# Kernel optimization log

Hardware: AMD Instinct MI355X
Metric: run time of the kernel (lower is better)

Reference implementation:

```python
import jax, jax.numpy as jnp
import numpy as np

# ---- static config (matches module defaults / init_kwargs) ----
SX = 256; SY = 256; C = 3; NK = 12; B = 4
R = 10; DT = 0.2; DD = 5; SIGMA = 0.65; THETA_A = 1.0; N_EXP = 2


def _build_kernels():
    """Replicates compute_kernel(): multi-ring Lenia kernels, normalized in real space."""
    rng = np.random.default_rng(42)
    mid = SX // 2
    g = np.mgrid[-mid:mid, -mid:mid]
    dist = np.linalg.norm(g, axis=0)  # [SX, SY]
    Ks = []
    for _ in range(NK):
        r = rng.uniform(0.3, 1.0)
        a = rng.uniform(0.0, 1.0, 3)
        w = rng.uniform(0.05, 0.2, 3)
        b = rng.uniform(0.0, 1.0, 3)
        D = dist / ((R + 15) * r)
        sig = 1.0 / (1.0 + np.exp((D - 1.0) * 10.0))  # sigmoid(-(D-1)*10)
        kerf = (b[None, None, :] * np.exp(-(((D[..., None] - a[None, None, :]) / w[None, None, :]) ** 2) / 2.0)).sum(-1)
        Ks.append(sig * kerf)
    K = np.stack(Ks, axis=-1)  # [SX, SY, NK]
    Kn = K / K.sum(axis=(0, 1), keepdims=True)
    m = rng.uniform(0.05, 0.5, NK)
    s = rng.uniform(0.01, 0.18, NK)
    h = rng.uniform(0.2, 1.0, NK)
    return (Kn.astype(np.float32), m.astype(np.float32), s.astype(np.float32), h.astype(np.float32))


def setup_inputs() -> dict:
    key = jax.random.key(0)
    Kn, m, s, h = _build_kernels()
    A = jax.random.uniform(key, (B, 1, SX, SY, C), dtype=jnp.float32)
    c0 = jnp.asarray(np.arange(NK) % C, dtype=jnp.int32)      # source channel of each kernel
    c1_map = jnp.asarray(np.arange(NK) % C, dtype=jnp.int32)  # target channel of each kernel
    return {"A": A, "Kn": jnp.asarray(Kn), "m": jnp.asarray(m), "s": jnp.asarray(s),
            "h": jnp.asarray(h), "c0": c0, "c1_map": c1_map}


def _sobel(A):
    """Circular (torus) Sobel, separable [1,2,1]x[-1,0,1]/8, on spatial axes (2,3).
    A: [B,1,SX,SY,C] -> [B,1,SX,SY,2,C] (d/dx, d/dy)."""
    sy = jnp.roll(A, -1, 3) + 2.0 * A + jnp.roll(A, 1, 3)
    gx = (jnp.roll(sy, -1, 2) - jnp.roll(sy, 1, 2)) / 8.0
    sx = jnp.roll(A, -1, 2) + 2.0 * A + jnp.roll(A, 1, 2)
    gy = (jnp.roll(sx, -1, 3) - jnp.roll(sx, 1, 3)) / 8.0
    return jnp.stack([gx, gy], axis=4)


def _forward(A, Kn, m, s, h, c0, c1_map):
    # FFT-domain convolution per kernel
    fK = jnp.fft.fft2(jnp.fft.fftshift(Kn, axes=(0, 1)), axes=(0, 1))  # [SX,SY,NK] complex
    fA = jnp.fft.fft2(A, axes=(2, 3))                                   # [B,1,SX,SY,C]
    fAk = fA[..., c0]                                                    # [B,1,SX,SY,NK]
    U = jnp.fft.ifft2(fK[None, None] * fAk, axes=(2, 3)).real           # [B,1,SX,SY,NK]
    # growth(U,m,s) = 2*bell(U,m,s)-1, scaled by h
    G = (2.0 * jnp.exp(-((U - m) ** 2) / (2.0 * s ** 2)) - 1.0) * h
    # sum kernel contributions into their target channel (c1)
    M = jax.nn.one_hot(c1_map, C, dtype=G.dtype)                         # [NK,C]
    Uc = jnp.einsum('bzxyk,kc->bzxyc', G, M)                             # [B,1,SX,SY,C]
    nabla_U = _sobel(Uc)                                                 # [B,1,SX,SY,2,C]
    nabla_A = _sobel(A.sum(-1, keepdims=True))                           # [B,1,SX,SY,2,1]
    alpha = jnp.clip((A[:, :, :, :, None, :] / THETA_A) ** N_EXP, 0.0, 1.0)
    F = nabla_U * (1.0 - alpha) - nabla_A * alpha                        # flow field
    # ---- reintegration tracking (RT) over a (2*DD+1)^2 neighborhood ----
    x = jnp.arange(SX, dtype=F.dtype); y = jnp.arange(SY, dtype=F.dtype)
    pos = jnp.stack(jnp.meshgrid(x, y, indexing='ij'), axis=-1) + 0.5    # [SX,SY,2]
    ma = DD - SIGMA
    mus = pos[None, None, :, :, :, None] + jnp.clip(DT * F, -ma, ma)     # target centers [B,1,SX,SY,2,C]
    offsets = jnp.asarray([(dx, dy) for dx in range(-DD, DD + 1) for dy in range(-DD, DD + 1)], dtype=jnp.int32)
    amax = min(1.0, 2.0 * SIGMA)

    def body(acc, off):
        dx, dy = off[0], off[1]
        rollA = jnp.roll(A, (dx, dy), axis=(2, 3))
        rollmu = jnp.roll(mus, (dx, dy), axis=(2, 3))
        dpmu = jnp.abs(pos[None, None, :, :, :, None] - rollmu)
        sz = 0.5 - dpmu + SIGMA
        area = jnp.prod(jnp.clip(sz, 0.0, amax), axis=4) / (4.0 * SIGMA ** 2)  # [B,1,SX,SY,C]
        return acc + rollA * area, None

    nA, _ = jax.lax.scan(jax.checkpoint(body), jnp.zeros_like(A), offsets)
    return nA


def reference(A, Kn, m, s, h, c0, c1_map):
    return _forward(A, Kn, m, s, h, c0, c1_map)
```

## Files before the change

### kernel.cpp

```cpp
#include <hip/hip_runtime.h>


typedef _Float16 f16;
typedef __attribute__((ext_vector_type(8))) _Float16 half8;
typedef __attribute__((ext_vector_type(16))) float f32x16;

#define RMAX 44
#define NROWS 89
#define NDMAX 8
#define NFRAG (3*NROWS*NDMAX)
#define NBPK ((NFRAG + 4) / 4)
#define ST 168
#define TROWS 120
#define SCHED_STRIDE 1024
#define KTHR 1e-7f

__global__ __launch_bounds__(128) void lenia_meta(const float* __restrict__ Kn,
                                                  int2* __restrict__ meta,
                                                  int* __restrict__ rowr) {
    int blk = blockIdx.x;
    int c = blk / NROWS, ri = blk - c * NROWS;
    int di = ri - RMAX;
    int t = threadIdx.x;
    int dj = t - RMAX;
    int act = 0;
    if (t < NROWS) {
        size_t base = (size_t)(((di + 128) << 8) | (dj + 128)) * 12 + c;
        float k0 = Kn[base], k1 = Kn[base + 3], k2 = Kn[base + 6], k3 = Kn[base + 9];
        act = (fmaxf(fmaxf(k0, k1), fmaxf(k2, k3)) > KTHR) ? 1 : 0;
    }
    __shared__ int smn[128], smx[128];
    smn[t] = act ? dj : 1000;
    smx[t] = act ? dj : -1000;
    __syncthreads();
    for (int s = 64; s > 0; s >>= 1) {
        if (t < s) { smn[t] = min(smn[t], smn[t + s]); smx[t] = max(smx[t], smx[t + s]); }
        __syncthreads();
    }
    if (t == 0) {
        int jmn = smn[0], jmx = smx[0];
        if (jmx < jmn) { meta[blk] = make_int2(1, 0); rowr[blk] = 0; }
        else {
            meta[blk] = make_int2(jmn, jmx);
            rowr[blk] = max(abs(di), max(abs(jmn), abs(jmx)));
        }
    }
}

__global__ __launch_bounds__(128) void lenia_sched(const int2* __restrict__ meta,
                                                   const int* __restrict__ rowr,
                                                   int2* __restrict__ meta2,
                                                   unsigned int* __restrict__ sched,
                                                   int* __restrict__ nsched,
                                                   int* __restrict__ radii) {
    int c = blockIdx.x;
    int t = threadIdx.x;
    __shared__ int pre[NROWS], nds[NROWS], rmx[128];
    int nd = 0, d0 = 0;
    if (t < NROWS) {
        int2 bm = meta[c * NROWS + t];
        if (bm.y >= bm.x) {
            d0 = ((bm.x - 7) >> 3) << 3;
            nd = ((bm.y + 7 - d0) >> 4) + 1;
        }
        meta2[c * NROWS + t] = make_int2(d0, nd);
        nds[t] = nd;
    }
    rmx[t] = (t < NROWS) ? rowr[c * NROWS + t] : 0;
    __syncthreads();
    for (int s = 64; s > 0; s >>= 1) {
        if (t < s) rmx[t] = max(rmx[t], rmx[t + s]);
        __syncthreads();
    }
    __shared__ int tot;
    if (t == 0) {
        radii[c] = rmx[0];
        int acc = 0;
        for (int i = 0; i < NROWS; ++i) { pre[i] = acc; acc += nds[i]; }
        tot = acc;
    }
    __syncthreads();
    if (t < NROWS && nd > 0) {
        int base = pre[t];
        for (int i = 0; i < nd; ++i) {
            int delta = d0 + 16 * i;
            unsigned int off = (unsigned int)(t * ST + delta + 128);
            sched[c * SCHED_STRIDE + base + i] =
                (unsigned int)((c * NROWS + t) * NDMAX + i) | (off << 12);
        }
    }
    if (t == 0) {
        int ns = (tot + 31) & ~31;
        unsigned int padoff = (unsigned int)(RMAX * ST + 128);
        for (int i = tot; i < ns + 48; ++i)
            sched[c * SCHED_STRIDE + i] = (unsigned int)NFRAG | (padoff << 12);
        nsched[c] = ns;
    }
}

__global__ __launch_bounds__(256) void lenia_prep2(const float* __restrict__ Kn,
                                                   const float* __restrict__ A,
                                                   const int2* __restrict__ meta2,
                                                   uint4* __restrict__ bpack,
                                                   f16* __restrict__ Atr) {
    int blk = blockIdx.x;
    if (blk < NBPK) {
        int fi = blk * 4 + (threadIdx.x >> 6);
        int l = threadIdx.x & 63;
        if (fi > NFRAG) return;
        union { f16 h[8]; uint4 u; } pk;
        if (fi == NFRAG) {
            pk.u = make_uint4(0, 0, 0, 0);
            bpack[(size_t)fi * 64 + l] = pk.u;
            return;
        }
        int c = fi / (NROWS * NDMAX);
        int rem = fi - c * (NROWS * NDMAX);
        int ri = rem >> 3, didx = rem & 7;
        int di = ri - RMAX;
        int delta = meta2[c * NROWS + ri].x + 16 * didx;
        int q = (l & 31) >> 3, sy = l & 7, g = l >> 5;
        int dj0 = delta + 8 * g - sy;
        const float* src = Kn + (size_t)(((di + 128) << 8) + (dj0 + 128)) * 12 + c + 3 * q;
        #pragma unroll
        for (int j = 0; j < 8; ++j) pk.h[j] = (f16)src[j * 12];
        bpack[(size_t)fi * 64 + l] = pk.u;
    } else {
        int px = (blk - NBPK) * 256 + threadIdx.x;
        int b = px >> 16, rem = px & 65535;
        const float* ap = A + (size_t)px * 3;
        Atr[(size_t)(b * 3 + 0) * 65536 + rem] = (f16)ap[0];
        Atr[(size_t)(b * 3 + 1) * 65536 + rem] = (f16)ap[1];
        Atr[(size_t)(b * 3 + 2) * 65536 + rem] = (f16)ap[2];
    }
}

__global__ __launch_bounds__(512, 6) void lenia_conv(
        const f16* __restrict__ Atr, const uint4* __restrict__ bpack,
        const unsigned int* __restrict__ sched, const int* __restrict__ nsched,
        const int* __restrict__ radii,
        const float* __restrict__ mp, const float* __restrict__ sp,
        const float* __restrict__ hp, f16* __restrict__ Uc) {
    extern __shared__ f16 smh[];

    const int tid = threadIdx.x;
    const int bc = blockIdx.y;
    const int b = bc / 3, c = bc - b * 3;
    const int x0 = (blockIdx.x >> 3) << 5;
    const int y0 = (blockIdx.x & 7) << 5;

    const int R = __builtin_amdgcn_readfirstlane(min(max(radii[c], 1), RMAX));
    const int R8 = (R + 7) & ~7;
    const int colbase = y0 - R8 - 16;
    const int rows = 32 + 2 * R;
    const f16* Ap = Atr + (size_t)(b * 3 + c) * 65536;

    {
        int nchunk = rows * 21;
        int tr = tid / 21, rem = tid - tr * 21;
        for (int ci = tid; ci < nchunk; ci += 512) {
            int gi = (x0 - R + tr) & 255;
            int gj = (colbase + rem * 8) & 255;
            *(half8*)(smh + tr * ST + rem * 8) = *(const half8*)(Ap + (gi << 8) + gj);
            tr += 24; rem += 8;
            if (rem >= 21) { rem -= 21; ++tr; }
        }
    }
    __syncthreads();

    const int lane = tid & 63, wid = tid >> 6;
    const int p = wid & 1, qr = wid >> 1;
    const int m = lane & 31, g = lane >> 5;
    const int abase = (m + R - RMAX) * ST + 16 * p + R8 + 16 + 8 * g - 128;

    const int ns = __builtin_amdgcn_readfirstlane(nsched[c]);
    const int nsQ = ns >> 2;
    const unsigned int* sW = sched + c * SCHED_STRIDE + qr * nsQ;

    f32x16 accA, accB;
    #pragma unroll
    for (int r = 0; r < 16; ++r) { accA[r] = 0.f; accB[r] = 0.f; }

    int eq[8];
    uint4 bq[8];
    #pragma unroll
    for (int j = 0; j < 8; ++j) {
        int e = __builtin_amdgcn_readfirstlane((int)sW[j]);
        eq[j] = e;
        bq[j] = bpack[(size_t)(e & 4095) * 64 + lane];
    }

    for (int it = 0; it < nsQ; it += 8) {
        #pragma unroll
        for (int j = 0; j < 8; ++j) {
            const int off = abase + (eq[j] >> 12);
            half8 a0 = *(const half8*)(smh + off);
            half8 a1 = *(const half8*)(smh + off + 8);
            union { uint4 u; half8 h; } bb; bb.u = bq[j];
            accA = __builtin_amdgcn_mfma_f32_32x32x16_f16(a0, bb.h, accA, 0, 0, 0);
            accB = __builtin_amdgcn_mfma_f32_32x32x16_f16(a1, bb.h, accB, 0, 0, 0);
            int ne = __builtin_amdgcn_readfirstlane((int)sW[it + 8 + j]);
            eq[j] = ne;
            bq[j] = bpack[(size_t)(ne & 4095) * 64 + lane];
        }
    }

    __syncthreads();
    float* red = (float*)smh;
    if (qr >= 2) {
        float* dst = red + ((size_t)(((p << 1) + (qr - 2)) * 64 + lane)) * 33;
        #pragma unroll
        for (int r = 0; r < 16; ++r) { dst[r] = accA[r]; dst[16 + r] = accB[r]; }
    }
    __syncthreads();
    if (qr < 2) {
        const float* src = red + ((size_t)(((p << 1) + qr) * 64 + lane)) * 33;
        #pragma unroll
        for (int r = 0; r < 16; ++r) { accA[r] += src[r]; accB[r] += src[16 + r]; }
    }
    __syncthreads();
    if (qr == 1) {
        float* dst = red + ((size_t)(p * 64 + lane)) * 33;
        #pragma unroll
        for (int r = 0; r < 16; ++r) { dst[r] = accA[r]; dst[16 + r] = accB[r]; }
    }
    __syncthreads();
    if (qr == 0) {
        const float* src = red + ((size_t)(p * 64 + lane)) * 33;
        #pragma unroll
        for (int r = 0; r < 16; ++r) { accA[r] += src[r]; accB[r] += src[16 + r]; }

        const int q = (lane & 31) >> 3, sy = lane & 7;
        const float mq = mp[c + 3 * q];
        const float sq = sp[c + 3 * q];
        const float hq = hp[c + 3 * q];
        const float i2s = 1.f / (2.f * sq * sq);
        #pragma unroll
        for (int oo = 0; oo < 2; ++oo) {
            const f32x16& acc = oo ? accB : accA;
            const int col = y0 + 16 * p + 8 * oo + sy;
            #pragma unroll
            for (int r = 0; r < 16; ++r) {
                float d = acc[r] - mq;
                float gg = (2.f * expf(-d * d * i2s) - 1.f) * hq;
                gg += __shfl_xor(gg, 8);
                gg += __shfl_xor(gg, 16);
                if ((lane & 24) == 0) {
                    int row = (r & 3) + ((r >> 2) << 3) + (g << 2);
                    Uc[((size_t)(b << 16) + ((x0 + row) << 8) + col) * 3 + c] = (f16)gg;
                }
            }
        }
    }
}

#define FTW 44
#define FSW 45
#define PLH (FSW * FTW)
__global__ __launch_bounds__(256) void lenia_flowrt(
        const f16* __restrict__ Atr, const f16* __restrict__ Uc,
        float* __restrict__ out) {
    extern __shared__ char fraw[];
    f16*    ucp = (f16*)fraw;
    f16*    atp = (f16*)(fraw + PLH * 2);
    float2* muq = (float2*)(fraw + 8 * PLH);

    int bc = blockIdx.y;
    int b = bc / 3, c = bc - b * 3;
    int t = blockIdx.x;
    int x0 = (t >> 3) << 5, y0 = (t & 7) << 5;
    const f16* A0 = Atr + (size_t)(b * 3) * 65536;
    const f16* Ub = Uc + ((size_t)b << 16) * 3;

    for (int idx = threadIdx.x; idx < FTW * FTW; idx += 256) {
        int si = idx / FTW, sj = idx - si * FTW;
        int gi = (x0 - 6 + si) & 255, gj = (y0 - 6 + sj) & 255;
        int pix = (gi << 8) + gj;
        int o = si * FSW + sj;
        ucp[o] = Ub[(size_t)pix * 3 + c];
        atp[o] = A0[pix];
        atp[PLH + o] = A0[65536 + pix];
        atp[2 * PLH + o] = A0[131072 + pix];
    }
    __syncthreads();

    for (int idx = threadIdx.x; idx < 42 * 42; idx += 256) {
        int ci = idx / 42, cj = idx - ci * 42;
        int si = ci + 1, sj = cj + 1;
        int o = si * FSW + sj;
        int vx = x0 - 6 + si, vy = y0 - 6 + sj;
        float sx = (vx < 0 || vx > 255) ? 1e7f : 0.f;
        float syv = (vy < 0 || vy > 255) ? 1e7f : 0.f;

        float as[3][3];
        #pragma unroll
        for (int i = 0; i < 3; ++i)
            #pragma unroll
            for (int j = 0; j < 3; ++j) {
                int oo = o + (i - 1) * FSW + (j - 1);
                as[i][j] = (float)atp[oo] + (float)atp[PLH + oo] + (float)atp[2 * PLH + oo];
            }
        float gxA = ((as[2][0] + 2.f * as[2][1] + as[2][2])
                   - (as[0][0] + 2.f * as[0][1] + as[0][2])) * 0.125f;
        float gyA = ((as[0][2] + 2.f * as[1][2] + as[2][2])
                   - (as[0][0] + 2.f * as[1][0] + as[2][0])) * 0.125f;

        float u00 = ucp[o - FSW - 1], u01 = ucp[o - FSW], u02 = ucp[o - FSW + 1];
        float u10 = ucp[o - 1],                          u12 = ucp[o + 1];
        float u20 = ucp[o + FSW - 1], u21 = ucp[o + FSW], u22 = ucp[o + FSW + 1];
        float gx = ((u20 + 2.f * u21 + u22) - (u00 + 2.f * u01 + u02)) * 0.125f;
        float gy = ((u02 + 2.f * u12 + u22) - (u00 + 2.f * u10 + u20)) * 0.125f;
        float a = (float)atp[c * PLH + o];
        float alpha = fminf(a * a, 1.f);
        float Fx = gx * (1.f - alpha) - gxA * alpha;
        float Fy = gy * (1.f - alpha) - gyA * alpha;
        float dx = fminf(fmaxf(0.2f * Fx, -4.35f), 4.35f) + sx;
        float dy = fminf(fmaxf(0.2f * Fy, -4.35f), 4.35f) + syv;
        muq[o] = make_float2(dx, dy);
    }
    __syncthreads();

    int tx = threadIdx.x & 31, tyg = threadIdx.x >> 5;
    int ty0 = tyg << 2;
    float a0 = 0.f, a1 = 0.f, a2 = 0.f, a3 = 0.f;
    const f16* ac = atp + c * PLH;

    for (int dxs = 0; dxs < 11; ++dxs) {
        float fdx = (float)(5 - dxs);
        int rowb = (tx + 1 + dxs) * FSW + (ty0 + 1);
        #pragma unroll
        for (int sjj = 0; sjj < 14; ++sjj) {
            float fdy = (float)(5 - sjj);
            float2 mu = muq[rowb + sjj];
            float av = (float)ac[rowb + sjj];
            float wx = fminf(fmaxf(1.15f - fabsf(fdx - mu.x), 0.f), 1.f);
            float awx = av * wx;
            float e0 = fdy - mu.y;
            a0 = fmaf(awx, fminf(fmaxf(1.15f - fabsf(e0), 0.f), 1.f), a0);
            a1 = fmaf(awx, fminf(fmaxf(1.15f - fabsf(e0 + 1.f), 0.f), 1.f), a1);
            a2 = fmaf(awx, fminf(fmaxf(1.15f - fabsf(e0 + 2.f), 0.f), 1.f), a2);
            a3 = fmaf(awx, fminf(fmaxf(1.15f - fabsf(e0 + 3.f), 0.f), 1.f), a3);
        }
    }
    const float inv = 1.0f / 1.69f;
    size_t ob = ((size_t)(b << 16) + ((x0 + tx) << 8) + (y0 + ty0)) * 3 + c;
    out[ob]     = a0 * inv;
    out[ob + 3] = a1 * inv;
    out[ob + 6] = a2 * inv;
    out[ob + 9] = a3 * inv;
}

extern "C" void kernel_launch(void* const* d_in, const int* in_sizes, int n_in,
                              void* d_out, int out_size, void* d_ws, size_t ws_size,
                              hipStream_t stream) {
    const float* A  = (const float*)d_in[0];
    const float* Kn = (const float*)d_in[1];
    const float* m  = (const float*)d_in[2];
    const float* s  = (const float*)d_in[3];
    const float* h  = (const float*)d_in[4];

    char* ws = (char*)d_ws;
    int*          radii = (int*)ws;
    int*          nschd = (int*)(ws + 16);
    int*          rowr  = (int*)(ws + 64);
    int2*         meta  = (int2*)(ws + 2048);
    int2*         meta2 = (int2*)(ws + 8192);
    unsigned int* sched = (unsigned int*)(ws + 16384);
    f16*          Atr   = (f16*)(ws + 32768);
    uint4*        bpack = (uint4*)(ws + 1605632);
    f16*          Uc    = (f16*)(ws + 3793920);

    lenia_meta<<<3 * NROWS, 128, 0, stream>>>(Kn, meta, rowr);
    lenia_sched<<<3, 128, 0, stream>>>(meta, rowr, meta2, sched, nschd, radii);
    lenia_prep2<<<NBPK + 1024, 256, 0, stream>>>(Kn, A, meta2, bpack, Atr);
    lenia_conv<<<dim3(64, 12), 512, TROWS * ST * sizeof(f16), stream>>>(
        Atr, bpack, sched, nschd, radii, m, s, h, Uc);
    lenia_flowrt<<<dim3(64, 12), 256, 8 * PLH + PLH * 8, stream>>>(
        Atr, Uc, (float*)d_out);
}
```

Measured before the change: 70.53 us.

## Halve conv tile width and split kernel schedule across eight waves

The conv kernel's output tile shrinks from 32x32 to 32x16 columns, which doubles the grid to 128x12 blocks and narrows the LDS row stride. All eight waves now cover the same 16 columns and each takes one eighth of the kernel-fragment schedule, instead of two column halves times four schedule quarters. Schedule padding rises to a multiple of 64 and the cross-wave reduction gains an extra level. The intent is more blocks for occupancy and a smaller LDS footprint, at the cost of more halo reloading per output, more B-fragment traffic and a deeper reduction.

New measurement: 82.11 us. 16.4% more time.

```diff
diff --git a/kernel.cpp b/kernel.cpp
--- a/kernel.cpp
+++ b/kernel.cpp
@@ -10,7 +10,7 @@
 #define NDMAX 8
 #define NFRAG (3*NROWS*NDMAX)
 #define NBPK ((NFRAG + 4) / 4)
-#define ST 168
+#define ST 152
 #define TROWS 120
 #define SCHED_STRIDE 1024
 #define KTHR 1e-7f
@@ -90,7 +90,7 @@
         }
     }
     if (t == 0) {
-        int ns = (tot + 31) & ~31;
+        int ns = (tot + 63) & ~63;
         unsigned int padoff = (unsigned int)(RMAX * ST + 128);
         for (int i = tot; i < ns + 48; ++i)
             sched[c * SCHED_STRIDE + i] = (unsigned int)NFRAG | (padoff << 12);
@@ -135,7 +135,7 @@
     }
 }
 
-__global__ __launch_bounds__(512, 6) void lenia_conv(
+__global__ __launch_bounds__(512, 8) void lenia_conv(
         const f16* __restrict__ Atr, const uint4* __restrict__ bpack,
         const unsigned int* __restrict__ sched, const int* __restrict__ nsched,
         const int* __restrict__ radii,
@@ -146,8 +146,9 @@
     const int tid = threadIdx.x;
     const int bc = blockIdx.y;
     const int b = bc / 3, c = bc - b * 3;
-    const int x0 = (blockIdx.x >> 3) << 5;
-    const int y0 = (blockIdx.x & 7) << 5;
+    const int t = blockIdx.x;
+    const int x0 = (t >> 4) << 5;
+    const int y0 = (t & 15) << 4;
 
     const int R = __builtin_amdgcn_readfirstlane(min(max(radii[c], 1), RMAX));
     const int R8 = (R + 7) & ~7;
@@ -156,26 +157,25 @@
     const f16* Ap = Atr + (size_t)(b * 3 + c) * 65536;
 
     {
-        int nchunk = rows * 21;
-        int tr = tid / 21, rem = tid - tr * 21;
+        int nchunk = rows * 19;
+        int tr = tid / 19, rem = tid - tr * 19;
         for (int ci = tid; ci < nchunk; ci += 512) {
             int gi = (x0 - R + tr) & 255;
             int gj = (colbase + rem * 8) & 255;
             *(half8*)(smh + tr * ST + rem * 8) = *(const half8*)(Ap + (gi << 8) + gj);
-            tr += 24; rem += 8;
-            if (rem >= 21) { rem -= 21; ++tr; }
-        }
-    }
-    __syncthreads();
-
-    const int lane = tid & 63, wid = tid >> 6;
-    const int p = wid & 1, qr = wid >> 1;
+            tr += 26; rem += 18;
+            if (rem >= 19) { rem -= 19; ++tr; }
+        }
+    }
+    __syncthreads();
+
+    const int lane = tid & 63, e = tid >> 6;
     const int m = lane & 31, g = lane >> 5;
-    const int abase = (m + R - RMAX) * ST + 16 * p + R8 + 16 + 8 * g - 128;
+    const int abase = (m + R - RMAX) * ST + R8 + 16 + 8 * g - 128;
 
     const int ns = __builtin_amdgcn_readfirstlane(nsched[c]);
-    const int nsQ = ns >> 2;
-    const unsigned int* sW = sched + c * SCHED_STRIDE + qr * nsQ;
+    const int nsE = ns >> 3;
+    const unsigned int* sW = sched + c * SCHED_STRIDE + e * nsE;
 
     f32x16 accA, accB;
     #pragma unroll
@@ -185,12 +185,12 @@
     uint4 bq[8];
     #pragma unroll
     for (int j = 0; j < 8; ++j) {
-        int e = __builtin_amdgcn_readfirstlane((int)sW[j]);
-        eq[j] = e;
-        bq[j] = bpack[(size_t)(e & 4095) * 64 + lane];
-    }
-
-    for (int it = 0; it < nsQ; it += 8) {
+        int ev = __builtin_amdgcn_readfirstlane((int)sW[j]);
+        eq[j] = ev;
+        bq[j] = bpack[(size_t)(ev & 4095) * 64 + lane];
+    }
+
+    for (int it = 0; it < nsE; it += 8) {
         #pragma unroll
         for (int j = 0; j < 8; ++j) {
             const int off = abase + (eq[j] >> 12);
@@ -205,28 +205,40 @@
         }
     }
 
-    __syncthreads();
     float* red = (float*)smh;
-    if (qr >= 2) {
-        float* dst = red + ((size_t)(((p << 1) + (qr - 2)) * 64 + lane)) * 33;
+    __syncthreads();
+    if (e >= 4) {
+        float* dst = red + ((size_t)((e - 4) * 64 + lane)) * 33;
         #pragma unroll
         for (int r = 0; r < 16; ++r) { dst[r] = accA[r]; dst[16 + r] = accB[r]; }
     }
     __syncthreads();
-    if (qr < 2) {
-        const float* src = red + ((size_t)(((p << 1) + qr) * 64 + lane)) * 33;
+    if (e < 4) {
+        const float* src = red + ((size_t)(e * 64 + lane)) * 33;
         #pragma unroll
         for (int r = 0; r < 16; ++r) { accA[r] += src[r]; accB[r] += src[16 + r]; }
     }
     __syncthreads();
-    if (qr == 1) {
-        float* dst = red + ((size_t)(p * 64 + lane)) * 33;
+    if (e == 2 || e == 3) {
+        float* dst = red + ((size_t)((e - 2) * 64 + lane)) * 33;
         #pragma unroll
         for (int r = 0; r < 16; ++r) { dst[r] = accA[r]; dst[16 + r] = accB[r]; }
     }
     __syncthreads();
-    if (qr == 0) {
-        const float* src = red + ((size_t)(p * 64 + lane)) * 33;
+    if (e < 2) {
+        const float* src = red + ((size_t)(e * 64 + lane)) * 33;
+        #pragma unroll
+        for (int r = 0; r < 16; ++r) { accA[r] += src[r]; accB[r] += src[16 + r]; }
+    }
+    __syncthreads();
+    if (e == 1) {
+        float* dst = red + (size_t)lane * 33;
+        #pragma unroll
+        for (int r = 0; r < 16; ++r) { dst[r] = accA[r]; dst[16 + r] = accB[r]; }
+    }
+    __syncthreads();
+    if (e == 0) {
+        const float* src = red + (size_t)lane * 33;
         #pragma unroll
         for (int r = 0; r < 16; ++r) { accA[r] += src[r]; accB[r] += src[16 + r]; }
 
@@ -238,7 +250,7 @@
         #pragma unroll
         for (int oo = 0; oo < 2; ++oo) {
             const f32x16& acc = oo ? accB : accA;
-            const int col = y0 + 16 * p + 8 * oo + sy;
+            const int col = y0 + 8 * oo + sy;
             #pragma unroll
             for (int r = 0; r < 16; ++r) {
                 float d = acc[r] - mq;
@@ -373,7 +385,7 @@
     lenia_meta<<<3 * NROWS, 128, 0, stream>>>(Kn, meta, rowr);
     lenia_sched<<<3, 128, 0, stream>>>(meta, rowr, meta2, sched, nschd, radii);
     lenia_prep2<<<NBPK + 1024, 256, 0, stream>>>(Kn, A, meta2, bpack, Atr);
-    lenia_conv<<<dim3(64, 12), 512, TROWS * ST * sizeof(f16), stream>>>(
+    lenia_conv<<<dim3(128, 12), 512, TROWS * ST * sizeof(f16), stream>>>(
         Atr, bpack, sched, nschd, radii, m, s, h, Uc);
     lenia_flowrt<<<dim3(64, 12), 256, 8 * PLH + PLH * 8, stream>>>(
         Atr, Uc, (float*)d_out);
```
